# Optimization experiments

Measured on AMD Instinct MI355X. Metric: run time of the kernel, lower is better.

## Reference

```python
import jax, jax.numpy as jnp
import numpy as np


def _ln(x, g, b, eps=1e-5):
    m = x.mean(-1, keepdims=True)
    v = x.var(-1, keepdims=True)
    return (x - m) / jnp.sqrt(v + eps) * g + b


def _causal_linear_attn(q, k, v, eps=1e-3):
    # q, k, v: (b, h, n, d). Matches lucidrains causal_linear_attn with bucket_size=1:
    # q -> softmax over feature dim, k -> exp, inclusive cumsum of k and k(outer)v over n.
    dh = q.shape[-1]
    q = jax.nn.softmax(q, axis=-1) * (dh ** -0.5)
    k = jnp.exp(k)
    k_cum = jnp.cumsum(k, axis=2)                                  # (b,h,n,d)
    ctx = jnp.cumsum(k[..., :, None] * v[..., None, :], axis=2)    # (b,h,n,d,d) running sum of k_i v_i^T
    d_inv = 1.0 / jnp.clip(jnp.einsum('bhnd,bhnd->bhn', k_cum, q), eps, None)
    return jnp.einsum('bhnd,bhnde->bhne', q, ctx) * d_inv[..., None]


def reference(x, ln1_g, ln1_b, Wq, Wk, Wv, Wo, bo, ln2_g, ln2_b, W1, b1, W2, b2, n_heads):
    depth = Wq.shape[0]
    B, N, D = x.shape
    H = int(n_heads)
    dh = D // H
    for i in range(depth):
        # --- pre-norm linear self-attention block ---
        xn = _ln(x, ln1_g[i], ln1_b[i])
        q = (xn @ Wq[i]).reshape(B, N, H, dh).transpose(0, 2, 1, 3)
        k = (xn @ Wk[i]).reshape(B, N, H, dh).transpose(0, 2, 1, 3)
        v = (xn @ Wv[i]).reshape(B, N, H, dh).transpose(0, 2, 1, 3)
        a = _causal_linear_attn(q, k, v)
        a = a.transpose(0, 2, 1, 3).reshape(B, N, D)
        x = x + a @ Wo[i] + bo[i]
        # --- pre-norm feed-forward block (mult=4, exact GELU) ---
        xn = _ln(x, ln2_g[i], ln2_b[i])
        x = x + jax.nn.gelu(xn @ W1[i] + b1[i], approximate=False) @ W2[i] + b2[i]
    return x


def setup_inputs() -> dict:
    key = jax.random.key(0)
    ks = jax.random.split(key, 8)
    B, N, D, H, depth = 2, 2048, 1024, 16, 2
    FF = 4 * D
    s = D ** -0.5
    x = jax.random.normal(ks[0], (B, N, D), dtype=jnp.float32)
    Wq = jax.random.normal(ks[1], (depth, D, D), dtype=jnp.float32) * s
    Wk = jax.random.normal(ks[2], (depth, D, D), dtype=jnp.float32) * s
    Wv = jax.random.normal(ks[3], (depth, D, D), dtype=jnp.float32) * s
    Wo = jax.random.normal(ks[4], (depth, D, D), dtype=jnp.float32) * s
    W1 = jax.random.normal(ks[5], (depth, D, FF), dtype=jnp.float32) * s
    W2 = jax.random.normal(ks[6], (depth, FF, D), dtype=jnp.float32) * (FF ** -0.5)
    return dict(
        x=x,
        ln1_g=jnp.ones((depth, D), jnp.float32), ln1_b=jnp.zeros((depth, D), jnp.float32),
        Wq=Wq, Wk=Wk, Wv=Wv, Wo=Wo, bo=jnp.zeros((depth, D), jnp.float32),
        ln2_g=jnp.ones((depth, D), jnp.float32), ln2_b=jnp.zeros((depth, D), jnp.float32),
        W1=W1, b1=jnp.zeros((depth, FF), jnp.float32),
        W2=W2, b2=jnp.zeros((depth, D), jnp.float32),
        n_heads=H,
    )
```

## Files before the change

### kernel.cpp

```cpp
#include <hip/hip_runtime.h>
#include <cmath>

#define BB 2
#define SEQ 2048
#define DIM 1024
#define NH 16
#define DH 64
#define DEPTH 2
#define FFD 4096
#define CHK 64
#define NCHK (SEQ/CHK)
#define ROWS (BB*SEQ)
#define QKP (3*DIM)

typedef __bf16 bf16x8 __attribute__((ext_vector_type(8)));
typedef __bf16 bf16x4 __attribute__((ext_vector_type(4)));
typedef float  f32x4  __attribute__((ext_vector_type(4)));

#define AS1 __attribute__((address_space(1)))
#define AS3 __attribute__((address_space(3)))
#define FENCE() asm volatile("" ::: "memory")
#define WAIT_LGKM0_NOPIN() asm volatile("s_waitcnt lgkmcnt(0)" ::: "memory")

__device__ __forceinline__ float gelu_fast(float x) {
    float x3 = x * x * x;
    float y = 1.5957691216057308f * (x + 0.044715f * x3);
    return x * __builtin_amdgcn_rcpf(1.0f + __expf(-y));
}

__device__ __forceinline__ int swz128(int row, int col) {
    return row * 64 + (col ^ ((row & 7) << 3));
}

__device__ __forceinline__ void swz_tile(int bid, int NX, int NY, int& tx, int& ty) {
    int NB = NX * NY;
    int q = NB >> 3, r = NB & 7;
    int xcd = bid & 7, seq = bid >> 3;
    int start = (xcd < r) ? xcd * (q + 1) : r * (q + 1) + (xcd - r) * q;
    int wgid = start + seq;
    int g = 0, rem = wgid;
    int gw = (NX < 4) ? NX : 4;
    while (rem >= gw * NY) {
        rem -= gw * NY; g++;
        int left = NX - 4 * g;
        gw = left < 4 ? left : 4;
    }
    ty = rem / gw;
    tx = 4 * g + rem % gw;
}

__global__ __launch_bounds__(256) void ln_kernel(
    const float* __restrict__ x, const float* __restrict__ g,
    const float* __restrict__ b, __bf16* __restrict__ out)
{
    int row = blockIdx.x;
    const float4* xr = (const float4*)(x + (size_t)row * DIM);
    int t = threadIdx.x;
    float4 v = xr[t];
    float s  = v.x + v.y + v.z + v.w;
    float ss = v.x*v.x + v.y*v.y + v.z*v.z + v.w*v.w;
    #pragma unroll
    for (int off = 32; off > 0; off >>= 1) {
        s  += __shfl_down(s, off);
        ss += __shfl_down(ss, off);
    }
    __shared__ float wsum[4], wsq[4], stats[2];
    int wid = t >> 6, lane = t & 63;
    if (lane == 0) { wsum[wid] = s; wsq[wid] = ss; }
    __syncthreads();
    if (t == 0) {
        float S  = wsum[0] + wsum[1] + wsum[2] + wsum[3];
        float SS = wsq[0] + wsq[1] + wsq[2] + wsq[3];
        float mean = S * (1.0f / DIM);
        float var  = SS * (1.0f / DIM) - mean * mean;
        stats[0] = mean;
        stats[1] = rsqrtf(var + 1e-5f);
    }
    __syncthreads();
    float mean = stats[0], rstd = stats[1];
    float4 gv = ((const float4*)g)[t];
    float4 bv = ((const float4*)b)[t];
    bf16x4 o;
    o[0] = (__bf16)((v.x - mean) * rstd * gv.x + bv.x);
    o[1] = (__bf16)((v.y - mean) * rstd * gv.y + bv.y);
    o[2] = (__bf16)((v.z - mean) * rstd * gv.z + bv.z);
    o[3] = (__bf16)((v.w - mean) * rstd * gv.w + bv.w);
    *(bf16x4*)(out + (size_t)row * DIM + t * 4) = o;
}

__global__ __launch_bounds__(256) void transpose_bf16(
    const float* __restrict__ W, __bf16* __restrict__ Wt, int K, int N)
{
    __shared__ float tile[32][33];
    int bx = blockIdx.x * 32;
    int by = blockIdx.y * 32;
    int tx = threadIdx.x & 31, ty = threadIdx.x >> 5;
    #pragma unroll
    for (int i = 0; i < 32; i += 8)
        tile[ty + i][tx] = W[(size_t)(by + ty + i) * N + bx + tx];
    __syncthreads();
    #pragma unroll
    for (int i = 0; i < 32; i += 8)
        Wt[(size_t)(bx + ty + i) * K + by + tx] = (__bf16)tile[tx][ty + i];
}

__global__ __launch_bounds__(256) void transpose_v(
    const __bf16* __restrict__ qkv, __bf16* __restrict__ vT)
{
    __shared__ __bf16 tile[64 * 64];
    int bx = blockIdx.x;
    int by = blockIdx.y;
    int t = threadIdx.x;
    int r0 = t >> 3, sl = t & 7;
    #pragma unroll
    for (int i = 0; i < 2; i++) {
        int row = i * 32 + r0;
        bf16x8 d = *(const bf16x8*)(qkv + (size_t)(bx * 64 + row) * QKP + 2 * DIM + by * 64 + sl * 8);
        *(bf16x8*)&tile[row * 64 + ((sl ^ (row & 7)) << 3)] = d;
    }
    __syncthreads();
    #pragma unroll
    for (int i = 0; i < 2; i++) {
        int d = i * 32 + r0;
        int rbase = sl * 8;
        bf16x8 o;
        #pragma unroll
        for (int j = 0; j < 8; j++) {
            int rr = rbase + j;
            o[j] = tile[rr * 64 + (((((d >> 3)) ^ (rr & 7)) << 3) | (d & 7))];
        }
        *(bf16x8*)(vT + (size_t)(by * 64 + d) * ROWS + bx * 64 + rbase) = o;
    }
}

#define GBM 128
#define GBN 128
#define GBK 64
template<int MODE, int OUTBF>
__global__ __launch_bounds__(256) void gemm_bf16(
    const __bf16* __restrict__ A, const __bf16* __restrict__ Bt,
    void* __restrict__ Cv, const float* __restrict__ bias,
    const float* __restrict__ res, int M, int N, int K, int NXT, int NYT)
{
    __shared__ __bf16 Als[GBM * GBK];
    __shared__ __bf16 Bls[GBN * GBK];
    int tx, ty;
    swz_tile(blockIdx.x, NXT, NYT, tx, ty);
    const int t = threadIdx.x;
    const int lane = t & 63;
    const int w = t >> 6;
    const int wr = w >> 1, wc = w & 1;
    const int bm = ty * GBM, bn = tx * GBN;

    f32x4 acc[4][4] = {};

    const int srow = w * 32 + (lane >> 3);
    const int scol = (lane & 7) * 8;
    const __bf16* gA = A + (size_t)(bm + srow) * K + scol;
    const __bf16* gB = Bt + (size_t)(bn + srow) * K + scol;
    __bf16* lA = Als + w * 2048;
    __bf16* lB = Bls + w * 2048;

    for (int k0 = 0; k0 < K; k0 += GBK) {
        #pragma unroll
        for (int i = 0; i < 4; i++) {
            __builtin_amdgcn_global_load_lds(
                (const AS1 void*)(gA + (size_t)(i * 8) * K + k0),
                (AS3 void*)(lA + i * 512), 16, 0, 0);
            __builtin_amdgcn_global_load_lds(
                (const AS1 void*)(gB + (size_t)(i * 8) * K + k0),
                (AS3 void*)(lB + i * 512), 16, 0, 0);
        }
        __syncthreads();
        #pragma unroll
        for (int kk = 0; kk < GBK; kk += 32) {
            bf16x8 af[4], bfr[4];
            #pragma unroll
            for (int m = 0; m < 4; m++)
                af[m] = *(const bf16x8*)&Als[(wr * 64 + m * 16 + (lane & 15)) * GBK + kk + (lane >> 4) * 8];
            #pragma unroll
            for (int n = 0; n < 4; n++)
                bfr[n] = *(const bf16x8*)&Bls[(wc * 64 + n * 16 + (lane & 15)) * GBK + kk + (lane >> 4) * 8];
            #pragma unroll
            for (int m = 0; m < 4; m++)
                #pragma unroll
                for (int n = 0; n < 4; n++)
                    acc[m][n] = __builtin_amdgcn_mfma_f32_16x16x32_bf16(af[m], bfr[n], acc[m][n], 0, 0, 0);
        }
        __syncthreads();
    }
    const int crow0 = bm + wr * 64 + (lane >> 4) * 4;
    const int ccol0 = bn + wc * 64 + (lane & 15);
    #pragma unroll
    for (int m = 0; m < 4; m++) {
        #pragma unroll
        for (int n = 0; n < 4; n++) {
            int col = ccol0 + n * 16;
            #pragma unroll
            for (int r = 0; r < 4; r++) {
                int row = crow0 + m * 16 + r;
                float v = acc[m][n][r];
                if (MODE == 1) v += res[(size_t)row * N + col] + bias[col];
                if (MODE == 2) v = gelu_fast(v + bias[col]);
                if (OUTBF) ((__bf16*)Cv)[(size_t)row * N + col] = (__bf16)v;
                else       ((float*)Cv)[(size_t)row * N + col] = v;
            }
        }
    }
}

#define TBM 256
#define TBN 256
#define TBK 64
template<int MODE, int OUTBF>
__global__ __launch_bounds__(512) void gemm256(
    const __bf16* __restrict__ A, const __bf16* __restrict__ Bt,
    void* __restrict__ Cv, const float* __restrict__ bias,
    const float* __restrict__ res, int M, int N, int K, int Kp,
    int NXT, int NYT, int NS)
{
    __shared__ __bf16 lds[2][2][TBM * TBK];
    int nb = NXT * NYT;
    int sk = blockIdx.x / nb;
    int tx, ty;
    swz_tile(blockIdx.x % nb, NXT, NYT, tx, ty);
    if (NS > 1) {
        A  += (size_t)sk * K;
        Bt += (size_t)sk * K;
        Cv = (void*)((char*)Cv + (size_t)sk * M * N * (OUTBF ? 2 : 4));
    }
    const int bm = ty * TBM, bn = tx * TBN;
    const int t = threadIdx.x;
    const int l = t & 63, w = t >> 6;
    const int wm = w >> 2, wn = w & 3;
    const int lm = l & 15, lk = l >> 4;

    f32x4 acc[8][4] = {};
    const int nt = K / TBK;
    const int NIT = nt / 2;

    auto STAGEH = [&](int bf, int mat, int hf, int kt) {
        const __bf16* src = mat ? Bt : A;
        int base = mat ? bn : bm;
        int k0 = kt * TBK;
        #pragma unroll
        for (int i = 0; i < 2; i++) {
            int row = hf * 128 + i * 64 + (t >> 3);
            int sl = (t & 7) ^ (row & 7);
            __builtin_amdgcn_global_load_lds(
                (const AS1 void*)(src + (size_t)(base + row) * Kp + k0 + sl * 8),
                (AS3 void*)(&lds[bf][mat][(hf * 2 + i) * 4096 + w * 512]), 16, 0, 0);
        }
    };
    auto LDA = [&](int bf, int g, bf16x8* af) {
        #pragma unroll
        for (int j = 0; j < 4; j++)
            #pragma unroll
            for (int kk = 0; kk < 2; kk++) {
                int row = wm * 128 + (g * 4 + j) * 16 + lm;
                int slot = kk * 4 + lk;
                af[j * 2 + kk] = *(const bf16x8*)&lds[bf][0][row * 64 + ((slot ^ (row & 7)) << 3)];
            }
    };
    auto LDB = [&](int bf, bf16x8* bfv) {
        #pragma unroll
        for (int n = 0; n < 4; n++)
            #pragma unroll
            for (int kk = 0; kk < 2; kk++) {
                int row = wn * 64 + n * 16 + lm;
                int slot = kk * 4 + lk;
                bfv[n * 2 + kk] = *(const bf16x8*)&lds[bf][1][row * 64 + ((slot ^ (row & 7)) << 3)];
            }
    };
    auto MM = [&](int g, int ng, bf16x8* af, bf16x8* bfv) {
        __builtin_amdgcn_s_setprio(1);
        #pragma unroll
        for (int j = 0; j < 4; j++)
            #pragma unroll
            for (int nn = 0; nn < 2; nn++)
                #pragma unroll
                for (int kk = 0; kk < 2; kk++)
                    acc[g * 4 + j][ng * 2 + nn] = __builtin_amdgcn_mfma_f32_16x16x32_bf16(
                        af[j * 2 + kk], bfv[(ng * 2 + nn) * 2 + kk], acc[g * 4 + j][ng * 2 + nn], 0, 0, 0);
        __builtin_amdgcn_s_setprio(0);
    };

    STAGEH(0, 0, 0, 0); STAGEH(0, 0, 1, 0); STAGEH(0, 1, 0, 0); STAGEH(0, 1, 1, 0);
    STAGEH(1, 1, 0, 1); STAGEH(1, 1, 1, 1); STAGEH(1, 0, 0, 1);
    asm volatile("s_waitcnt vmcnt(6)" ::: "memory");
    __builtin_amdgcn_s_barrier();

    bf16x8 aF[8], bF[8];
    for (int it = 0; it < NIT; it++) {
        int T2 = 2 * it + 2, U2 = 2 * it + 3;
        LDA(0, 0, aF); LDB(0, bF);
        STAGEH(1, 0, 1, 2 * it + 1);
        FENCE(); __builtin_amdgcn_s_barrier();
        MM(0, 0, aF, bF);
        WAIT_LGKM0_NOPIN();
        FENCE(); __builtin_amdgcn_s_barrier();
        if (T2 < nt) STAGEH(0, 1, 0, T2);
        FENCE(); __builtin_amdgcn_s_barrier();
        MM(0, 1, aF, bF);
        FENCE(); __builtin_amdgcn_s_barrier();
        LDA(0, 1, aF);
        if (T2 < nt) STAGEH(0, 1, 1, T2);
        FENCE(); __builtin_amdgcn_s_barrier();
        MM(1, 1, aF, bF);
        FENCE(); __builtin_amdgcn_s_barrier();
        if (T2 < nt) {
            STAGEH(0, 0, 0, T2);
            asm volatile("s_waitcnt vmcnt(6)" ::: "memory");
        } else {
            asm volatile("s_waitcnt vmcnt(0)" ::: "memory");
        }
        __builtin_amdgcn_s_barrier();
        MM(1, 0, aF, bF);
        FENCE(); __builtin_amdgcn_s_barrier();
        LDA(1, 0, aF); LDB(1, bF);
        if (T2 < nt) STAGEH(0, 0, 1, T2);
        FENCE(); __builtin_amdgcn_s_barrier();
        MM(0, 0, aF, bF);
        WAIT_LGKM0_NOPIN();
        FENCE(); __builtin_amdgcn_s_barrier();
        if (U2 < nt) STAGEH(1, 1, 0, U2);
        FENCE(); __builtin_amdgcn_s_barrier();
        MM(0, 1, aF, bF);
        FENCE(); __builtin_amdgcn_s_barrier();
        LDA(1, 1, aF);
        if (U2 < nt) STAGEH(1, 1, 1, U2);
        FENCE(); __builtin_amdgcn_s_barrier();
        MM(1, 1, aF, bF);
        FENCE(); __builtin_amdgcn_s_barrier();
        if (U2 < nt) {
            STAGEH(1, 0, 0, U2);
            asm volatile("s_waitcnt vmcnt(6)" ::: "memory");
        } else {
            asm volatile("s_waitcnt vmcnt(0)" ::: "memory");
        }
        __builtin_amdgcn_s_barrier();
        MM(1, 0, aF, bF);
        FENCE(); __builtin_amdgcn_s_barrier();
    }

    #pragma unroll
    for (int m = 0; m < 8; m++) {
        #pragma unroll
        for (int n = 0; n < 4; n++) {
            int col = bn + wn * 64 + n * 16 + lm;
            #pragma unroll
            for (int r = 0; r < 4; r++) {
                int row = bm + wm * 128 + m * 16 + lk * 4 + r;
                float v = acc[m][n][r];
                if (MODE == 1) v += res[(size_t)row * N + col] + bias[col];
                if (MODE == 2) v = gelu_fast(v + bias[col]);
                if (OUTBF) ((__bf16*)Cv)[(size_t)row * N + col] = (__bf16)v;
                else       ((float*)Cv)[(size_t)row * N + col] = v;
            }
        }
    }
}

__global__ __launch_bounds__(256) void reduce4(
    const __bf16* __restrict__ parts, const float* __restrict__ bias,
    float* __restrict__ x)
{
    const size_t PS = (size_t)ROWS * DIM;
    int idx = blockIdx.x * 256 + threadIdx.x;
    float4 xr = ((const float4*)x)[idx];
    float4 bv = ((const float4*)bias)[idx & (DIM / 4 - 1)];
    float o0 = xr.x + bv.x, o1 = xr.y + bv.y, o2 = xr.z + bv.z, o3 = xr.w + bv.w;
    #pragma unroll
    for (int s = 0; s < 4; s++) {
        bf16x4 p = *(const bf16x4*)(parts + s * PS + (size_t)idx * 4);
        o0 += (float)p[0]; o1 += (float)p[1]; o2 += (float)p[2]; o3 += (float)p[3];
    }
    float4 o = {o0, o1, o2, o3};
    ((float4*)x)[idx] = o;
}

__global__ __launch_bounds__(256) void attn_local_m(
    const __bf16* __restrict__ qkv, const __bf16* __restrict__ vTg,
    float* __restrict__ KVT, float* __restrict__ Ksum)
{
    int blk = blockIdx.x;
    int c = blk % NCHK, bh = blk / NCHK;
    int b = bh / NH, h = bh % NH;
    __shared__ __bf16 ek_s[64 * 64];
    __shared__ __bf16 ekT_s[64 * 68];
    __shared__ float ksum_p[4][64];
    int t = threadIdx.x, w = t >> 6, l = t & 63;
    size_t rowbase = (size_t)(b * SEQ + c * CHK);

    {
        int m = t >> 2, dq = t & 3;
        const __bf16* kr = qkv + (rowbase + m) * QKP + DIM + h * DH + dq * 16;
        bf16x8 k0 = *(const bf16x8*)kr;
        bf16x8 k1 = *(const bf16x8*)(kr + 8);
        bf16x8 e0, e1;
        #pragma unroll
        for (int j = 0; j < 8; j++) {
            e0[j] = (__bf16)__expf((float)k0[j]);
            e1[j] = (__bf16)__expf((float)k1[j]);
        }
        *(bf16x8*)&ek_s[swz128(m, dq * 16)] = e0;
        *(bf16x8*)&ek_s[swz128(m, dq * 16 + 8)] = e1;
    }
    __syncthreads();
    {
        float kacc = 0.f;
        #pragma unroll
        for (int g = 0; g < 4; g++) {
            bf16x4 pk;
            #pragma unroll
            for (int j = 0; j < 4; j++) {
                __bf16 e = ek_s[swz128(w * 16 + g * 4 + j, l)];
                pk[j] = e;
                kacc += (float)e;
            }
            *(bf16x4*)&ekT_s[l * 68 + w * 16 + g * 4] = pk;
        }
        ksum_p[w][l] = kacc;
    }
    __syncthreads();
    f32x4 acc[4] = {};
    const __bf16* vbase = vTg + (size_t)(h * DH + w * 16 + (l & 15)) * ROWS
                        + (size_t)b * SEQ + c * CHK + (l >> 4) * 8;
    bf16x8 a0 = *(const bf16x8*)vbase;
    bf16x8 a1 = *(const bf16x8*)(vbase + 32);
    #pragma unroll
    for (int fn = 0; fn < 4; fn++) {
        int rbase = (fn * 16 + (l & 15)) * 68 + (l >> 4) * 8;
        bf16x4 b0a = *(const bf16x4*)&ekT_s[rbase];
        bf16x4 b0b = *(const bf16x4*)&ekT_s[rbase + 4];
        bf16x4 b1a = *(const bf16x4*)&ekT_s[rbase + 32];
        bf16x4 b1b = *(const bf16x4*)&ekT_s[rbase + 36];
        bf16x8 b0, b1;
        #pragma unroll
        for (int j = 0; j < 4; j++) {
            b0[j] = b0a[j]; b0[j + 4] = b0b[j];
            b1[j] = b1a[j]; b1[j + 4] = b1b[j];
        }
        acc[fn] = __builtin_amdgcn_mfma_f32_16x16x32_bf16(a0, b0, acc[fn], 0, 0, 0);
        acc[fn] = __builtin_amdgcn_mfma_f32_16x16x32_bf16(a1, b1, acc[fn], 0, 0, 0);
    }
    float* kvout = KVT + (size_t)(bh * NCHK + c) * (DH * DH);
    #pragma unroll
    for (int fn = 0; fn < 4; fn++)
        #pragma unroll
        for (int r = 0; r < 4; r++)
            kvout[(w * 16 + (l >> 4) * 4 + r) * DH + fn * 16 + (l & 15)] = acc[fn][r];
    if (t < 64) {
        float s = ksum_p[0][t] + ksum_p[1][t] + ksum_p[2][t] + ksum_p[3][t];
        Ksum[(size_t)(bh * NCHK + c) * DH + t] = s;
    }
}

__global__ __launch_bounds__(256) void attn_scan2(
    float* __restrict__ KV, float* __restrict__ Ksum)
{
    int bh = blockIdx.y;
    int bx = blockIdx.x;
    int t = threadIdx.x;
    if (bx < 16) {
        int elem = bx * 256 + t;
        float run = 0.f;
        for (int c = 0; c < NCHK; c++) {
            float* p = KV + ((size_t)(bh * NCHK + c)) * (DH * DH) + elem;
            float tmp = *p;
            *p = run;
            run += tmp;
        }
    } else if (t < DH) {
        float run = 0.f;
        for (int c = 0; c < NCHK; c++) {
            float* p = Ksum + ((size_t)(bh * NCHK + c)) * DH + t;
            float tmp = *p;
            *p = run;
            run += tmp;
        }
    }
}

__global__ __launch_bounds__(256) void attn_out_m(
    const __bf16* __restrict__ qkv, const __bf16* __restrict__ vTg,
    const float* __restrict__ KVT, const float* __restrict__ Ksum,
    __bf16* __restrict__ ag)
{
    int blk = blockIdx.x;
    int c = blk % NCHK, bh = blk / NCHK;
    int b = bh / NH, h = bh % NH;
    __shared__ __bf16 q_s[64 * 64];
    __shared__ __bf16 ek_s[64 * 64];
    __shared__ __bf16 s_s[64 * 64];
    __shared__ __bf16 kvT_s[64 * 64];
    __shared__ float denom_s[64];
    int t = threadIdx.x, w = t >> 6, l = t & 63;
    size_t rowbase = (size_t)(b * SEQ + c * CHK);

    {
        int i = t >> 2, dq = t & 3;
        const __bf16* qr = qkv + (rowbase + i) * QKP + h * DH + dq * 16;
        bf16x8 q0 = *(const bf16x8*)qr, q1 = *(const bf16x8*)(qr + 8);
        float qf[16];
        #pragma unroll
        for (int j = 0; j < 8; j++) { qf[j] = (float)q0[j]; qf[8 + j] = (float)q1[j]; }
        float mx = qf[0];
        #pragma unroll
        for (int j = 1; j < 16; j++) mx = fmaxf(mx, qf[j]);
        mx = fmaxf(mx, __shfl_xor(mx, 1));
        mx = fmaxf(mx, __shfl_xor(mx, 2));
        float ss = 0.f;
        #pragma unroll
        for (int j = 0; j < 16; j++) { qf[j] = __expf(qf[j] - mx); ss += qf[j]; }
        ss += __shfl_xor(ss, 1);
        ss += __shfl_xor(ss, 2);
        float sc = 0.125f / ss;
        bf16x8 o0, o1;
        #pragma unroll
        for (int j = 0; j < 8; j++) {
            o0[j] = (__bf16)(qf[j] * sc);
            o1[j] = (__bf16)(qf[8 + j] * sc);
        }
        *(bf16x8*)&q_s[swz128(i, dq * 16)] = o0;
        *(bf16x8*)&q_s[swz128(i, dq * 16 + 8)] = o1;
        const float* kp = Ksum + (size_t)(bh * NCHK + c) * DH + dq * 16;
        float dk = 0.f;
        #pragma unroll
        for (int j = 0; j < 16; j++) dk += (qf[j] * sc) * kp[j];
        dk += __shfl_xor(dk, 1);
        dk += __shfl_xor(dk, 2);
        if (dq == 0) denom_s[i] = dk;
    }
    {
        int m = t >> 2, dq = t & 3;
        const __bf16* kr = qkv + (rowbase + m) * QKP + DIM + h * DH + dq * 16;
        bf16x8 k0 = *(const bf16x8*)kr, k1 = *(const bf16x8*)(kr + 8);
        bf16x8 e0, e1;
        #pragma unroll
        for (int j = 0; j < 8; j++) {
            e0[j] = (__bf16)__expf((float)k0[j]);
            e1[j] = (__bf16)__expf((float)k1[j]);
        }
        *(bf16x8*)&ek_s[swz128(m, dq * 16)] = e0;
        *(bf16x8*)&ek_s[swz128(m, dq * 16 + 8)] = e1;
    }
    {
        int e = t >> 2, dq = t & 3;
        const float* kvr = KVT + (size_t)(bh * NCHK + c) * (DH * DH) + e * DH + dq * 16;
        bf16x8 o0, o1;
        #pragma unroll
        for (int j = 0; j < 8; j++) { o0[j] = (__bf16)kvr[j]; o1[j] = (__bf16)kvr[8 + j]; }
        *(bf16x8*)&kvT_s[swz128(e, dq * 16)] = o0;
        *(bf16x8*)&kvT_s[swz128(e, dq * 16 + 8)] = o1;
    }
    __syncthreads();

    bf16x8 bq0 = *(const bf16x8*)&q_s[swz128(w * 16 + (l & 15), (l >> 4) * 8)];
    bf16x8 bq1 = *(const bf16x8*)&q_s[swz128(w * 16 + (l & 15), 32 + (l >> 4) * 8)];
    int i_col = w * 16 + (l & 15);
    float dsum = 0.f;
    #pragma unroll
    for (int fm = 0; fm < 4; fm++) {
        bf16x8 ae0 = *(const bf16x8*)&ek_s[swz128(fm * 16 + (l & 15), (l >> 4) * 8)];
        bf16x8 ae1 = *(const bf16x8*)&ek_s[swz128(fm * 16 + (l & 15), 32 + (l >> 4) * 8)];
        f32x4 z = {};
        z = __builtin_amdgcn_mfma_f32_16x16x32_bf16(ae0, bq0, z, 0, 0, 0);
        z = __builtin_amdgcn_mfma_f32_16x16x32_bf16(ae1, bq1, z, 0, 0, 0);
        bf16x4 pk;
        #pragma unroll
        for (int r = 0; r < 4; r++) {
            int m = fm * 16 + (l >> 4) * 4 + r;
            float v = (m <= i_col) ? z[r] : 0.f;
            pk[r] = (__bf16)v;
            dsum += (float)pk[r];
        }
        *(bf16x4*)&s_s[swz128(i_col, fm * 16 + (l >> 4) * 4)] = pk;
    }
    dsum += __shfl_xor(dsum, 16);
    dsum += __shfl_xor(dsum, 32);
    if (l < 16) denom_s[w * 16 + l] += dsum;

    bf16x8 as0 = *(const bf16x8*)&s_s[swz128(w * 16 + (l & 15), (l >> 4) * 8)];
    bf16x8 as1 = *(const bf16x8*)&s_s[swz128(w * 16 + (l & 15), 32 + (l >> 4) * 8)];
    f32x4 oacc[4] = {};
    #pragma unroll
    for (int fn = 0; fn < 4; fn++) {
        const __bf16* vb = vTg + (size_t)(h * DH + fn * 16 + (l & 15)) * ROWS
                         + (size_t)b * SEQ + c * CHK + (l >> 4) * 8;
        bf16x8 bv0 = *(const bf16x8*)vb;
        bf16x8 bv1 = *(const bf16x8*)(vb + 32);
        bf16x8 bk0 = *(const bf16x8*)&kvT_s[swz128(fn * 16 + (l & 15), (l >> 4) * 8)];
        bf16x8 bk1 = *(const bf16x8*)&kvT_s[swz128(fn * 16 + (l & 15), 32 + (l >> 4) * 8)];
        f32x4 z = oacc[fn];
        z = __builtin_amdgcn_mfma_f32_16x16x32_bf16(as0, bv0, z, 0, 0, 0);
        z = __builtin_amdgcn_mfma_f32_16x16x32_bf16(as1, bv1, z, 0, 0, 0);
        z = __builtin_amdgcn_mfma_f32_16x16x32_bf16(bq0, bk0, z, 0, 0, 0);
        z = __builtin_amdgcn_mfma_f32_16x16x32_bf16(bq1, bk1, z, 0, 0, 0);
        oacc[fn] = z;
    }
    #pragma unroll
    for (int r = 0; r < 4; r++) {
        int i = w * 16 + (l >> 4) * 4 + r;
        float dinv = 1.0f / fmaxf(denom_s[i], 1e-3f);
        #pragma unroll
        for (int fn = 0; fn < 4; fn++)
            ag[(rowbase + i) * DIM + h * DH + fn * 16 + (l & 15)] = (__bf16)(oacc[fn][r] * dinv);
    }
}

extern "C" void kernel_launch(void* const* d_in, const int* in_sizes, int n_in,
                              void* d_out, int out_size, void* d_ws, size_t ws_size,
                              hipStream_t stream) {
    (void)in_sizes; (void)n_in; (void)out_size; (void)ws_size;
    const float* x_in  = (const float*)d_in[0];
    const float* ln1_g = (const float*)d_in[1];
    const float* ln1_b = (const float*)d_in[2];
    const float* Wq    = (const float*)d_in[3];
    const float* Wk    = (const float*)d_in[4];
    const float* Wv    = (const float*)d_in[5];
    const float* Wo    = (const float*)d_in[6];
    const float* bo    = (const float*)d_in[7];
    const float* ln2_g = (const float*)d_in[8];
    const float* ln2_b = (const float*)d_in[9];
    const float* W1    = (const float*)d_in[10];
    const float* b1    = (const float*)d_in[11];
    const float* W2    = (const float*)d_in[12];
    const float* b2    = (const float*)d_in[13];

    float* x = (float*)d_out;
    const size_t MB = 1024 * 1024;
    char* base = (char*)d_ws;

    __bf16* qkv   = (__bf16*)base;
    __bf16* vTg   = (__bf16*)(base + 24 * MB);
    __bf16* h1    = (__bf16*)base;
    __bf16* xn    = (__bf16*)(base + 32 * MB);
    __bf16* parts = (__bf16*)(base + 32 * MB);
    __bf16* a     = (__bf16*)(base + 40 * MB);
    float*  KVT   = (float*)(base + 48 * MB);
    float*  Ks    = (float*)(base + 64 * MB);
    __bf16* wqkt  = (__bf16*)(base + 65 * MB);
    __bf16* wot   = (__bf16*)(base + 71 * MB);
    __bf16* w1t   = (__bf16*)(base + 73 * MB);
    __bf16* w2t   = (__bf16*)(base + 81 * MB);

    const size_t SZ = (size_t)ROWS * DIM;
    hipMemcpyAsync(x, x_in, SZ * sizeof(float), hipMemcpyDeviceToDevice, stream);

    dim3 gTd(DIM / 32, DIM / 32);
    dim3 gT1(FFD / 32, DIM / 32);
    dim3 gT2(DIM / 32, FFD / 32);
    dim3 gScan(17, BB * NH);
    dim3 gTv(ROWS / 64, DIM / 64);

    for (int l = 0; l < DEPTH; l++) {
        const float* wq = Wq + (size_t)l * DIM * DIM;
        const float* wk = Wk + (size_t)l * DIM * DIM;
        const float* wv = Wv + (size_t)l * DIM * DIM;
        const float* wo = Wo + (size_t)l * DIM * DIM;
        const float* w1 = W1 + (size_t)l * DIM * FFD;
        const float* w2 = W2 + (size_t)l * FFD * DIM;

        transpose_bf16<<<gTd, 256, 0, stream>>>(wq, wqkt, DIM, DIM);
        transpose_bf16<<<gTd, 256, 0, stream>>>(wk, wqkt + (size_t)DIM * DIM, DIM, DIM);
        transpose_bf16<<<gTd, 256, 0, stream>>>(wv, wqkt + 2 * (size_t)DIM * DIM, DIM, DIM);
        transpose_bf16<<<gTd, 256, 0, stream>>>(wo, wot, DIM, DIM);
        transpose_bf16<<<gT1, 256, 0, stream>>>(w1, w1t, DIM, FFD);
        transpose_bf16<<<gT2, 256, 0, stream>>>(w2, w2t, FFD, DIM);

        ln_kernel<<<ROWS, 256, 0, stream>>>(x, ln1_g + l * DIM, ln1_b + l * DIM, xn);
        gemm256<0, 1><<<12 * 16, 512, 0, stream>>>(xn, wqkt, qkv, nullptr, nullptr,
                                                   ROWS, QKP, DIM, DIM, 12, 16, 1);
        transpose_v<<<gTv, 256, 0, stream>>>(qkv, vTg);
        attn_local_m<<<BB * NH * NCHK, 256, 0, stream>>>(qkv, vTg, KVT, Ks);
        attn_scan2<<<gScan, 256, 0, stream>>>(KVT, Ks);
        attn_out_m<<<BB * NH * NCHK, 256, 0, stream>>>(qkv, vTg, KVT, Ks, a);
        gemm_bf16<1, 0><<<8 * 32, 256, 0, stream>>>(a, wot, x, bo + l * DIM, x,
                                                    ROWS, DIM, DIM, 8, 32);

        ln_kernel<<<ROWS, 256, 0, stream>>>(x, ln2_g + l * DIM, ln2_b + l * DIM, xn);
        gemm256<2, 1><<<16 * 16, 512, 0, stream>>>(xn, w1t, h1, b1 + l * FFD, nullptr,
                                                   ROWS, FFD, DIM, DIM, 16, 16, 1);
        gemm256<0, 1><<<4 * 16 * 4, 512, 0, stream>>>(h1, w2t, parts, nullptr, nullptr,
                                                      ROWS, DIM, FFD / 4, FFD, 4, 16, 4);
        reduce4<<<ROWS * DIM / 4 / 256, 256, 0, stream>>>(parts, b2 + l * DIM, x);
    }
}
```

Before: 432.8 us.

## Fuse weight transposes, split-K Wo GEMM, and fold LayerNorm into reductions

Merges the six per-layer weight transposes into a single launch and hoists LDS/global address math out of the 256-tile GEMM inner loops. The output projection now uses the 256-tile GEMM with 4-way split-K, replacing the old 128-tile kernel. The residual+bias reduction also computes the next LayerNorm, removing separate LN passes. This adds extra bf16 partial-sum traffic and reduces the residual add precision slightly via bf16 partials.

```diff
diff --git a/kernel.cpp b/kernel.cpp
--- a/kernel.cpp
+++ b/kernel.cpp
@@ -88,12 +88,34 @@
     *(bf16x4*)(out + (size_t)row * DIM + t * 4) = o;
 }
 
-__global__ __launch_bounds__(256) void transpose_bf16(
-    const float* __restrict__ W, __bf16* __restrict__ Wt, int K, int N)
-{
+__global__ __launch_bounds__(256) void transpose_all(
+    const float* __restrict__ wq, const float* __restrict__ wk,
+    const float* __restrict__ wv, const float* __restrict__ wo,
+    const float* __restrict__ w1, const float* __restrict__ w2,
+    __bf16* __restrict__ wqkt, __bf16* __restrict__ wot,
+    __bf16* __restrict__ w1t, __bf16* __restrict__ w2t)
+{
+    int id = blockIdx.x;
+    const float* W; __bf16* Wt; int K, N, txt, tyt;
+    if (id < 4096) {
+        int seg = id >> 10, r = id & 1023;
+        K = DIM; N = DIM;
+        txt = r & 31; tyt = r >> 5;
+        W  = seg == 0 ? wq : seg == 1 ? wk : seg == 2 ? wv : wo;
+        Wt = seg < 3 ? wqkt + (size_t)seg * DIM * DIM : wot;
+    } else if (id < 8192) {
+        int r = id - 4096;
+        K = DIM; N = FFD;
+        txt = r & 127; tyt = r >> 7;
+        W = w1; Wt = w1t;
+    } else {
+        int r = id - 8192;
+        K = FFD; N = DIM;
+        txt = r & 31; tyt = r >> 5;
+        W = w2; Wt = w2t;
+    }
     __shared__ float tile[32][33];
-    int bx = blockIdx.x * 32;
-    int by = blockIdx.y * 32;
+    int bx = txt * 32, by = tyt * 32;
     int tx = threadIdx.x & 31, ty = threadIdx.x >> 5;
     #pragma unroll
     for (int i = 0; i < 32; i += 8)
@@ -130,82 +152,6 @@
             o[j] = tile[rr * 64 + (((((d >> 3)) ^ (rr & 7)) << 3) | (d & 7))];
         }
         *(bf16x8*)(vT + (size_t)(by * 64 + d) * ROWS + bx * 64 + rbase) = o;
-    }
-}
-
-#define GBM 128
-#define GBN 128
-#define GBK 64
-template<int MODE, int OUTBF>
-__global__ __launch_bounds__(256) void gemm_bf16(
-    const __bf16* __restrict__ A, const __bf16* __restrict__ Bt,
-    void* __restrict__ Cv, const float* __restrict__ bias,
-    const float* __restrict__ res, int M, int N, int K, int NXT, int NYT)
-{
-    __shared__ __bf16 Als[GBM * GBK];
-    __shared__ __bf16 Bls[GBN * GBK];
-    int tx, ty;
-    swz_tile(blockIdx.x, NXT, NYT, tx, ty);
-    const int t = threadIdx.x;
-    const int lane = t & 63;
-    const int w = t >> 6;
-    const int wr = w >> 1, wc = w & 1;
-    const int bm = ty * GBM, bn = tx * GBN;
-
-    f32x4 acc[4][4] = {};
-
-    const int srow = w * 32 + (lane >> 3);
-    const int scol = (lane & 7) * 8;
-    const __bf16* gA = A + (size_t)(bm + srow) * K + scol;
-    const __bf16* gB = Bt + (size_t)(bn + srow) * K + scol;
-    __bf16* lA = Als + w * 2048;
-    __bf16* lB = Bls + w * 2048;
-
-    for (int k0 = 0; k0 < K; k0 += GBK) {
-        #pragma unroll
-        for (int i = 0; i < 4; i++) {
-            __builtin_amdgcn_global_load_lds(
-                (const AS1 void*)(gA + (size_t)(i * 8) * K + k0),
-                (AS3 void*)(lA + i * 512), 16, 0, 0);
-            __builtin_amdgcn_global_load_lds(
-                (const AS1 void*)(gB + (size_t)(i * 8) * K + k0),
-                (AS3 void*)(lB + i * 512), 16, 0, 0);
-        }
-        __syncthreads();
-        #pragma unroll
-        for (int kk = 0; kk < GBK; kk += 32) {
-            bf16x8 af[4], bfr[4];
-            #pragma unroll
-            for (int m = 0; m < 4; m++)
-                af[m] = *(const bf16x8*)&Als[(wr * 64 + m * 16 + (lane & 15)) * GBK + kk + (lane >> 4) * 8];
-            #pragma unroll
-            for (int n = 0; n < 4; n++)
-                bfr[n] = *(const bf16x8*)&Bls[(wc * 64 + n * 16 + (lane & 15)) * GBK + kk + (lane >> 4) * 8];
-            #pragma unroll
-            for (int m = 0; m < 4; m++)
-                #pragma unroll
-                for (int n = 0; n < 4; n++)
-                    acc[m][n] = __builtin_amdgcn_mfma_f32_16x16x32_bf16(af[m], bfr[n], acc[m][n], 0, 0, 0);
-        }
-        __syncthreads();
-    }
-    const int crow0 = bm + wr * 64 + (lane >> 4) * 4;
-    const int ccol0 = bn + wc * 64 + (lane & 15);
-    #pragma unroll
-    for (int m = 0; m < 4; m++) {
-        #pragma unroll
-        for (int n = 0; n < 4; n++) {
-            int col = ccol0 + n * 16;
-            #pragma unroll
-            for (int r = 0; r < 4; r++) {
-                int row = crow0 + m * 16 + r;
-                float v = acc[m][n][r];
-                if (MODE == 1) v += res[(size_t)row * N + col] + bias[col];
-                if (MODE == 2) v = gelu_fast(v + bias[col]);
-                if (OUTBF) ((__bf16*)Cv)[(size_t)row * N + col] = (__bf16)v;
-                else       ((float*)Cv)[(size_t)row * N + col] = v;
-            }
-        }
     }
 }
 
@@ -239,38 +185,44 @@
     const int nt = K / TBK;
     const int NIT = nt / 2;
 
+    const int s7 = lm & 7;
+    const int c0 = (lk ^ s7) << 3;
+    const int c1 = ((4 ^ lk) ^ s7) << 3;
+    const __bf16* pA[2][2] = {
+        { &lds[0][0][(wm * 128 + lm) * 64 + c0], &lds[0][0][(wm * 128 + lm) * 64 + c1] },
+        { &lds[1][0][(wm * 128 + lm) * 64 + c0], &lds[1][0][(wm * 128 + lm) * 64 + c1] } };
+    const __bf16* pB[2][2] = {
+        { &lds[0][1][(wn * 64 + lm) * 64 + c0], &lds[0][1][(wn * 64 + lm) * 64 + c1] },
+        { &lds[1][1][(wn * 64 + lm) * 64 + c0], &lds[1][1][(wn * 64 + lm) * 64 + c1] } };
+
+    const int srow0 = t >> 3;
+    const int scol0 = ((t & 7) ^ (srow0 & 7)) * 8;
+    const __bf16* gAb = A + (size_t)(bm + srow0) * Kp + scol0;
+    const __bf16* gBb = Bt + (size_t)(bn + srow0) * Kp + scol0;
+    const int ldsw = w * 512;
+
     auto STAGEH = [&](int bf, int mat, int hf, int kt) {
-        const __bf16* src = mat ? Bt : A;
-        int base = mat ? bn : bm;
-        int k0 = kt * TBK;
+        const __bf16* srcb = mat ? gBb : gAb;
         #pragma unroll
         for (int i = 0; i < 2; i++) {
-            int row = hf * 128 + i * 64 + (t >> 3);
-            int sl = (t & 7) ^ (row & 7);
             __builtin_amdgcn_global_load_lds(
-                (const AS1 void*)(src + (size_t)(base + row) * Kp + k0 + sl * 8),
-                (AS3 void*)(&lds[bf][mat][(hf * 2 + i) * 4096 + w * 512]), 16, 0, 0);
+                (const AS1 void*)(srcb + (size_t)(hf * 128 + i * 64) * Kp + kt * 64),
+                (AS3 void*)(&lds[bf][mat][(hf * 2 + i) * 4096 + ldsw]), 16, 0, 0);
         }
     };
     auto LDA = [&](int bf, int g, bf16x8* af) {
         #pragma unroll
-        for (int j = 0; j < 4; j++)
-            #pragma unroll
-            for (int kk = 0; kk < 2; kk++) {
-                int row = wm * 128 + (g * 4 + j) * 16 + lm;
-                int slot = kk * 4 + lk;
-                af[j * 2 + kk] = *(const bf16x8*)&lds[bf][0][row * 64 + ((slot ^ (row & 7)) << 3)];
-            }
+        for (int j = 0; j < 4; j++) {
+            af[j * 2 + 0] = *(const bf16x8*)(pA[bf][0] + (g * 4 + j) * 1024);
+            af[j * 2 + 1] = *(const bf16x8*)(pA[bf][1] + (g * 4 + j) * 1024);
+        }
     };
     auto LDB = [&](int bf, bf16x8* bfv) {
         #pragma unroll
-        for (int n = 0; n < 4; n++)
-            #pragma unroll
-            for (int kk = 0; kk < 2; kk++) {
-                int row = wn * 64 + n * 16 + lm;
-                int slot = kk * 4 + lk;
-                bfv[n * 2 + kk] = *(const bf16x8*)&lds[bf][1][row * 64 + ((slot ^ (row & 7)) << 3)];
-            }
+        for (int n = 0; n < 4; n++) {
+            bfv[n * 2 + 0] = *(const bf16x8*)(pB[bf][0] + n * 1024);
+            bfv[n * 2 + 1] = *(const bf16x8*)(pB[bf][1] + n * 1024);
+        }
     };
     auto MM = [&](int g, int ng, bf16x8* af, bf16x8* bfv) {
         __builtin_amdgcn_s_setprio(1);
@@ -361,22 +313,56 @@
     }
 }
 
-__global__ __launch_bounds__(256) void reduce4(
+template<int DOLN>
+__global__ __launch_bounds__(256) void reduce4ln(
     const __bf16* __restrict__ parts, const float* __restrict__ bias,
-    float* __restrict__ x)
+    float* __restrict__ x, const float* __restrict__ g,
+    const float* __restrict__ b, __bf16* __restrict__ xn)
 {
     const size_t PS = (size_t)ROWS * DIM;
-    int idx = blockIdx.x * 256 + threadIdx.x;
-    float4 xr = ((const float4*)x)[idx];
-    float4 bv = ((const float4*)bias)[idx & (DIM / 4 - 1)];
+    int row = blockIdx.x, t = threadIdx.x;
+    size_t base = (size_t)row * DIM + t * 4;
+    float4 xr = *(const float4*)(x + base);
+    float4 bv = ((const float4*)bias)[t];
     float o0 = xr.x + bv.x, o1 = xr.y + bv.y, o2 = xr.z + bv.z, o3 = xr.w + bv.w;
     #pragma unroll
     for (int s = 0; s < 4; s++) {
-        bf16x4 p = *(const bf16x4*)(parts + s * PS + (size_t)idx * 4);
+        bf16x4 p = *(const bf16x4*)(parts + s * PS + base);
         o0 += (float)p[0]; o1 += (float)p[1]; o2 += (float)p[2]; o3 += (float)p[3];
     }
     float4 o = {o0, o1, o2, o3};
-    ((float4*)x)[idx] = o;
+    *(float4*)(x + base) = o;
+    if constexpr (DOLN) {
+        float s  = o0 + o1 + o2 + o3;
+        float ss = o0*o0 + o1*o1 + o2*o2 + o3*o3;
+        #pragma unroll
+        for (int off = 32; off > 0; off >>= 1) {
+            s  += __shfl_down(s, off);
+            ss += __shfl_down(ss, off);
+        }
+        __shared__ float wsum[4], wsq[4], stats[2];
+        int wid = t >> 6, lane = t & 63;
+        if (lane == 0) { wsum[wid] = s; wsq[wid] = ss; }
+        __syncthreads();
+        if (t == 0) {
+            float S  = wsum[0] + wsum[1] + wsum[2] + wsum[3];
+            float SS = wsq[0] + wsq[1] + wsq[2] + wsq[3];
+            float mean = S * (1.0f / DIM);
+            float var  = SS * (1.0f / DIM) - mean * mean;
+            stats[0] = mean;
+            stats[1] = rsqrtf(var + 1e-5f);
+        }
+        __syncthreads();
+        float mean = stats[0], rstd = stats[1];
+        float4 gv = ((const float4*)g)[t];
+        float4 bvv = ((const float4*)b)[t];
+        bf16x4 on;
+        on[0] = (__bf16)((o0 - mean) * rstd * gv.x + bvv.x);
+        on[1] = (__bf16)((o1 - mean) * rstd * gv.y + bvv.y);
+        on[2] = (__bf16)((o2 - mean) * rstd * gv.z + bvv.z);
+        on[3] = (__bf16)((o3 - mean) * rstd * gv.w + bvv.w);
+        *(bf16x4*)(xn + base) = on;
+    }
 }
 
 __global__ __launch_bounds__(256) void attn_local_m(
@@ -632,25 +618,23 @@
     const size_t MB = 1024 * 1024;
     char* base = (char*)d_ws;
 
-    __bf16* qkv   = (__bf16*)base;
-    __bf16* vTg   = (__bf16*)(base + 24 * MB);
-    __bf16* h1    = (__bf16*)base;
-    __bf16* xn    = (__bf16*)(base + 32 * MB);
-    __bf16* parts = (__bf16*)(base + 32 * MB);
-    __bf16* a     = (__bf16*)(base + 40 * MB);
-    float*  KVT   = (float*)(base + 48 * MB);
-    float*  Ks    = (float*)(base + 64 * MB);
-    __bf16* wqkt  = (__bf16*)(base + 65 * MB);
-    __bf16* wot   = (__bf16*)(base + 71 * MB);
-    __bf16* w1t   = (__bf16*)(base + 73 * MB);
-    __bf16* w2t   = (__bf16*)(base + 81 * MB);
+    __bf16* qkv    = (__bf16*)base;
+    __bf16* partsO = (__bf16*)base;
+    __bf16* h1     = (__bf16*)base;
+    __bf16* vTg    = (__bf16*)(base + 24 * MB);
+    __bf16* xn     = (__bf16*)(base + 32 * MB);
+    __bf16* parts  = (__bf16*)(base + 32 * MB);
+    __bf16* a      = (__bf16*)(base + 40 * MB);
+    float*  KVT    = (float*)(base + 48 * MB);
+    float*  Ks     = (float*)(base + 64 * MB);
+    __bf16* wqkt   = (__bf16*)(base + 65 * MB);
+    __bf16* wot    = (__bf16*)(base + 71 * MB);
+    __bf16* w1t    = (__bf16*)(base + 73 * MB);
+    __bf16* w2t    = (__bf16*)(base + 81 * MB);
 
     const size_t SZ = (size_t)ROWS * DIM;
     hipMemcpyAsync(x, x_in, SZ * sizeof(float), hipMemcpyDeviceToDevice, stream);
 
-    dim3 gTd(DIM / 32, DIM / 32);
-    dim3 gT1(FFD / 32, DIM / 32);
-    dim3 gT2(DIM / 32, FFD / 32);
     dim3 gScan(17, BB * NH);
     dim3 gTv(ROWS / 64, DIM / 64);
 
@@ -662,28 +646,32 @@
         const float* w1 = W1 + (size_t)l * DIM * FFD;
         const float* w2 = W2 + (size_t)l * FFD * DIM;
 
-        transpose_bf16<<<gTd, 256, 0, stream>>>(wq, wqkt, DIM, DIM);
-        transpose_bf16<<<gTd, 256, 0, stream>>>(wk, wqkt + (size_t)DIM * DIM, DIM, DIM);
-        transpose_bf16<<<gTd, 256, 0, stream>>>(wv, wqkt + 2 * (size_t)DIM * DIM, DIM, DIM);
-        transpose_bf16<<<gTd, 256, 0, stream>>>(wo, wot, DIM, DIM);
-        transpose_bf16<<<gT1, 256, 0, stream>>>(w1, w1t, DIM, FFD);
-        transpose_bf16<<<gT2, 256, 0, stream>>>(w2, w2t, FFD, DIM);
-
-        ln_kernel<<<ROWS, 256, 0, stream>>>(x, ln1_g + l * DIM, ln1_b + l * DIM, xn);
+        transpose_all<<<12288, 256, 0, stream>>>(wq, wk, wv, wo, w1, w2,
+                                                 wqkt, wot, w1t, w2t);
+
+        if (l == 0)
+            ln_kernel<<<ROWS, 256, 0, stream>>>(x, ln1_g, ln1_b, xn);
         gemm256<0, 1><<<12 * 16, 512, 0, stream>>>(xn, wqkt, qkv, nullptr, nullptr,
                                                    ROWS, QKP, DIM, DIM, 12, 16, 1);
         transpose_v<<<gTv, 256, 0, stream>>>(qkv, vTg);
         attn_local_m<<<BB * NH * NCHK, 256, 0, stream>>>(qkv, vTg, KVT, Ks);
         attn_scan2<<<gScan, 256, 0, stream>>>(KVT, Ks);
         attn_out_m<<<BB * NH * NCHK, 256, 0, stream>>>(qkv, vTg, KVT, Ks, a);
-        gemm_bf16<1, 0><<<8 * 32, 256, 0, stream>>>(a, wot, x, bo + l * DIM, x,
-                                                    ROWS, DIM, DIM, 8, 32);
-
-        ln_kernel<<<ROWS, 256, 0, stream>>>(x, ln2_g + l * DIM, ln2_b + l * DIM, xn);
+        gemm256<0, 1><<<4 * 16 * 4, 512, 0, stream>>>(a, wot, partsO, nullptr, nullptr,
+                                                      ROWS, DIM, DIM / 4, DIM, 4, 16, 4);
+        reduce4ln<1><<<ROWS, 256, 0, stream>>>(partsO, bo + l * DIM, x,
+                                               ln2_g + l * DIM, ln2_b + l * DIM, xn);
+
         gemm256<2, 1><<<16 * 16, 512, 0, stream>>>(xn, w1t, h1, b1 + l * FFD, nullptr,
                                                    ROWS, FFD, DIM, DIM, 16, 16, 1);
         gemm256<0, 1><<<4 * 16 * 4, 512, 0, stream>>>(h1, w2t, parts, nullptr, nullptr,
                                                       ROWS, DIM, FFD / 4, FFD, 4, 16, 4);
-        reduce4<<<ROWS * DIM / 4 / 256, 256, 0, stream>>>(parts, b2 + l * DIM, x);
-    }
-}
+        if (l + 1 < DEPTH)
+            reduce4ln<1><<<ROWS, 256, 0, stream>>>(parts, b2 + l * DIM, x,
+                                                   ln1_g + (l + 1) * DIM,
+                                                   ln1_b + (l + 1) * DIM, xn);
+        else
+            reduce4ln<0><<<ROWS, 256, 0, stream>>>(parts, b2 + l * DIM, x,
+                                                   nullptr, nullptr, nullptr);
+    }
+}
```

New measurement: 399.2 us. 1.08x faster.
